# Optimization experiments

Hardware: AMD Instinct MI355X
Metric: run time of the kernel (lower is better)

## Reference

```python
import jax, jax.numpy as jnp
import numpy as np

EPS = 1e-8

def setup_inputs() -> dict:
    key = jax.random.key(0)
    k1, k2 = jax.random.split(key)
    B, C, H, W = 8, 21, 512, 512
    inp = jax.random.normal(k1, (B, C, H, W), dtype=jnp.float32)
    target = jax.random.uniform(k2, (B, C, H, W), dtype=jnp.float32)
    return {"input": inp, "target": target}

def reference(input, target):
    B, C, H, W = input.shape
    # argmax over class dim -> [B, H, W]
    pred = jnp.argmax(input, axis=1)
    # one-hot of prediction, flattened over spatial dims -> [B, HW, C]
    h = jax.nn.one_hot(pred.reshape(B, H * W), C, dtype=input.dtype)
    # target flattened over spatial dims -> [B, C, HW]
    y = target.reshape(B, C, H * W)
    # cm[b, i, j] = sum_n y[b, i, n] * h[b, n, j]  -> [B, C, C]
    cm = jnp.einsum('bin,bnj->bij', y, h)
    # row-normalize by target mass per class, then mean over batch -> [C, C]
    cm = cm / (jnp.sum(y, axis=2, keepdims=True) + EPS)
    return jnp.mean(cm, axis=0)
```

## Files before the change

### kernel.cpp

```cpp
#include <hip/hip_runtime.h>
#include <math.h>

#define NC 21
#define NB 8
#define HW (512*512)
#define EPS 1e-8f
#define NREP 8
#define TPB 256
#define G4 2
#define F4_PER_BLOCK (TPB * G4)
#define TILES_PER_IMG (HW / 4 / F4_PER_BLOCK)
#define NBLK (NB * TILES_PER_IMG)
#define PSTRIDE 512

typedef float f32x4 __attribute__((ext_vector_type(4)));


#define UPD(val, cc, mm, jj) \
    if ((val) > (mm) || ((val) == (mm) && (cc) < (jj))) { (mm) = (val); (jj) = (cc); }

template <bool PARTIAL>
__global__ __launch_bounds__(TPB) void cm_accum(const float* __restrict__ input,
                                                const float* __restrict__ target,
                                                float* __restrict__ cm ,
                                                float* __restrict__ partial ) {
    __shared__ float scm[NREP][NC * NC];
    const int t = threadIdx.x;
    for (int i = t; i < NREP * NC * NC; i += TPB) ((float*)scm)[i] = 0.0f;
    __syncthreads();

    const int bid  = blockIdx.x;
    const int b    = bid / TILES_PER_IMG;
    const int tile = bid % TILES_PER_IMG;
    const int rot  = bid % NC;

    const f32x4* ip = (const f32x4*)(input  + (size_t)b * NC * HW);
    const f32x4* tp = (const f32x4*)(target + (size_t)b * NC * HW);
    const int plane4 = HW / 4;
    const int q0 = tile * F4_PER_BLOCK + t;

    f32x4 mA, mB;
    mA.x = mA.y = mA.z = mA.w = -INFINITY;
    mB.x = mB.y = mB.z = mB.w = -INFINITY;
    int jAx = NC, jAy = NC, jAz = NC, jAw = NC;
    int jBx = NC, jBy = NC, jBz = NC, jBw = NC;

    int c = rot;
    f32x4 curA = __builtin_nontemporal_load(ip + (size_t)c * plane4 + q0);
    f32x4 curB = __builtin_nontemporal_load(ip + (size_t)c * plane4 + q0 + TPB);
    f32x4 nxtA = {}, nxtB = {};
    for (int cc = 0; cc < NC; ++cc) {
        const int cn = (c + 1 == NC) ? 0 : c + 1;
        if (cc < NC - 1) {
            nxtA = __builtin_nontemporal_load(ip + (size_t)cn * plane4 + q0);
            nxtB = __builtin_nontemporal_load(ip + (size_t)cn * plane4 + q0 + TPB);
        }
        __builtin_amdgcn_sched_barrier(0);
        UPD(curA.x, c, mA.x, jAx); UPD(curA.y, c, mA.y, jAy);
        UPD(curA.z, c, mA.z, jAz); UPD(curA.w, c, mA.w, jAw);
        UPD(curB.x, c, mB.x, jBx); UPD(curB.y, c, mB.y, jBy);
        UPD(curB.z, c, mB.z, jBz); UPD(curB.w, c, mB.w, jBw);
        curA = nxtA; curB = nxtB;
        c = cn;
    }

    float* my = scm[t & (NREP - 1)];
    c = rot;
    curA = __builtin_nontemporal_load(tp + (size_t)c * plane4 + q0);
    curB = __builtin_nontemporal_load(tp + (size_t)c * plane4 + q0 + TPB);
    for (int cc = 0; cc < NC; ++cc) {
        const int cn = (c + 1 == NC) ? 0 : c + 1;
        if (cc < NC - 1) {
            nxtA = __builtin_nontemporal_load(tp + (size_t)cn * plane4 + q0);
            nxtB = __builtin_nontemporal_load(tp + (size_t)cn * plane4 + q0 + TPB);
        }
        __builtin_amdgcn_sched_barrier(0);
        const int row = c * NC;
        atomicAdd(&my[row + jAx], curA.x);
        atomicAdd(&my[row + jAy], curA.y);
        atomicAdd(&my[row + jAz], curA.z);
        atomicAdd(&my[row + jAw], curA.w);
        atomicAdd(&my[row + jBx], curB.x);
        atomicAdd(&my[row + jBy], curB.y);
        atomicAdd(&my[row + jBz], curB.z);
        atomicAdd(&my[row + jBw], curB.w);
        curA = nxtA; curB = nxtB;
        c = cn;
    }
    __syncthreads();

    if (PARTIAL) {
        float* pout = partial + (size_t)bid * PSTRIDE;
        for (int i = t; i < PSTRIDE; i += TPB) {
            float s = 0.0f;
            if (i < NC * NC) {
                #pragma unroll
                for (int r = 0; r < NREP; ++r) s += scm[r][i];
            }
            pout[i] = s;
        }
    } else {
        for (int i = t; i < NC * NC; i += TPB) {
            float s = 0.0f;
            #pragma unroll
            for (int r = 0; r < NREP; ++r) s += scm[r][i];
            atomicAdd(&cm[b * NC * NC + i], s);
        }
    }
}

__global__ __launch_bounds__(256) void cm_reduce(const float* __restrict__ partial,
                                                 float* __restrict__ cm) {
    const int b = blockIdx.x, t = threadIdx.x;
    const float* p = partial + (size_t)b * TILES_PER_IMG * PSTRIDE;
    float s0 = 0.0f, s1 = 0.0f;
    #pragma unroll 8
    for (int s = 0; s < TILES_PER_IMG; ++s) {
        s0 += p[(size_t)s * PSTRIDE + t];
        s1 += p[(size_t)s * PSTRIDE + t + 256];
    }
    cm[b * NC * NC + t] = s0;
    if (t + 256 < NC * NC) cm[b * NC * NC + t + 256] = s1;
}

__global__ __launch_bounds__(512) void cm_final(const float* __restrict__ cm,
                                                float* __restrict__ out) {
    __shared__ float rs[NB * NC];
    const int t = threadIdx.x;
    if (t < NB * NC) {
        const int b = t / NC, i = t % NC;
        float s = 0.0f;
        for (int j = 0; j < NC; ++j) s += cm[b * NC * NC + i * NC + j];
        rs[t] = s + EPS;
    }
    __syncthreads();
    if (t < NC * NC) {
        const int i = t / NC;
        float acc = 0.0f;
        for (int b = 0; b < NB; ++b) acc += cm[b * NC * NC + t] / rs[b * NC + i];
        out[t] = acc * (1.0f / NB);
    }
}

extern "C" void kernel_launch(void* const* d_in, const int* in_sizes, int n_in,
                              void* d_out, int out_size, void* d_ws, size_t ws_size,
                              hipStream_t stream) {
    const float* input  = (const float*)d_in[0];
    const float* target = (const float*)d_in[1];
    float* out = (float*)d_out;

    const size_t partial_floats = (size_t)NBLK * PSTRIDE;
    const size_t need = (partial_floats + NB * NC * NC) * sizeof(float);

    if (ws_size >= need) {
        float* partial = (float*)d_ws;
        float* cm      = partial + partial_floats;
        cm_accum<true><<<NBLK, TPB, 0, stream>>>(input, target, cm, partial);
        cm_reduce<<<NB, 256, 0, stream>>>(partial, cm);
        cm_final<<<1, 512, 0, stream>>>(cm, out);
    } else {
        float* cm = (float*)d_ws;
        hipMemsetAsync(cm, 0, NB * NC * NC * sizeof(float), stream);
        cm_accum<false><<<NBLK, TPB, 0, stream>>>(input, target, cm, nullptr);
        cm_final<<<1, 512, 0, stream>>>(cm, out);
    }
}
```

Measured before the change: 516.4 us.

## Stage input and target planes into LDS via global_load_lds in chunks

Replaces per-thread register-prefetched nontemporal vector loads with direct global-to-LDS staging of all 21 class planes per 128-float4 chunk, processing four chunks per block. Each thread then reads two floats per class from LDS for the argmax and the atomic accumulation, and the number of shared histogram replicas is halved. This aims to raise memory-level parallelism by issuing all planes at once, but it adds a full vmcnt(0) wait plus several block barriers per chunk, which serializes loading and compute and removes the old overlap.

```diff
diff --git a/kernel.cpp b/kernel.cpp
--- a/kernel.cpp
+++ b/kernel.cpp
@@ -5,11 +5,12 @@
 #define NB 8
 #define HW (512*512)
 #define EPS 1e-8f
-#define NREP 8
+#define NREP 4
 #define TPB 256
-#define G4 2
-#define F4_PER_BLOCK (TPB * G4)
-#define TILES_PER_IMG (HW / 4 / F4_PER_BLOCK)
+#define CHUNK4 128
+#define CHUNKS_PER_BLK 4
+#define BLK4 (CHUNK4 * CHUNKS_PER_BLK)
+#define TILES_PER_IMG ((HW/4) / BLK4)
 #define NBLK (NB * TILES_PER_IMG)
 #define PSTRIDE 512
 
@@ -19,75 +20,68 @@
 #define UPD(val, cc, mm, jj) \
     if ((val) > (mm) || ((val) == (mm) && (cc) < (jj))) { (mm) = (val); (jj) = (cc); }
 
+__device__ __forceinline__ void stage_plane(const f32x4* gsrc, f32x4* lds_uniform, int lane) {
+    __builtin_amdgcn_global_load_lds(
+        (const __attribute__((address_space(1))) void*)(gsrc + lane),
+        (__attribute__((address_space(3))) void*)(uintptr_t)lds_uniform,
+        16, 0, 0);
+    __builtin_amdgcn_global_load_lds(
+        (const __attribute__((address_space(1))) void*)(gsrc + 64 + lane),
+        (__attribute__((address_space(3))) void*)(uintptr_t)(lds_uniform + 64),
+        16, 0, 0);
+}
+
 template <bool PARTIAL>
 __global__ __launch_bounds__(TPB) void cm_accum(const float* __restrict__ input,
                                                 const float* __restrict__ target,
                                                 float* __restrict__ cm ,
                                                 float* __restrict__ partial ) {
+    __shared__ f32x4 stage[NC][CHUNK4];
     __shared__ float scm[NREP][NC * NC];
     const int t = threadIdx.x;
+    const int wave = t >> 6, lane = t & 63;
     for (int i = t; i < NREP * NC * NC; i += TPB) ((float*)scm)[i] = 0.0f;
-    __syncthreads();
 
     const int bid  = blockIdx.x;
     const int b    = bid / TILES_PER_IMG;
     const int tile = bid % TILES_PER_IMG;
-    const int rot  = bid % NC;
-
     const f32x4* ip = (const f32x4*)(input  + (size_t)b * NC * HW);
     const f32x4* tp = (const f32x4*)(target + (size_t)b * NC * HW);
     const int plane4 = HW / 4;
-    const int q0 = tile * F4_PER_BLOCK + t;
 
-    f32x4 mA, mB;
-    mA.x = mA.y = mA.z = mA.w = -INFINITY;
-    mB.x = mB.y = mB.z = mB.w = -INFINITY;
-    int jAx = NC, jAy = NC, jAz = NC, jAw = NC;
-    int jBx = NC, jBy = NC, jBz = NC, jBw = NC;
+    for (int ch = 0; ch < CHUNKS_PER_BLK; ++ch) {
+        const int q0 = tile * BLK4 + ch * CHUNK4;
 
-    int c = rot;
-    f32x4 curA = __builtin_nontemporal_load(ip + (size_t)c * plane4 + q0);
-    f32x4 curB = __builtin_nontemporal_load(ip + (size_t)c * plane4 + q0 + TPB);
-    f32x4 nxtA = {}, nxtB = {};
-    for (int cc = 0; cc < NC; ++cc) {
-        const int cn = (c + 1 == NC) ? 0 : c + 1;
-        if (cc < NC - 1) {
-            nxtA = __builtin_nontemporal_load(ip + (size_t)cn * plane4 + q0);
-            nxtB = __builtin_nontemporal_load(ip + (size_t)cn * plane4 + q0 + TPB);
+        for (int c = wave; c < NC; c += 4)
+            stage_plane(ip + (size_t)c * plane4 + q0, &stage[c][0], lane);
+        asm volatile("s_waitcnt vmcnt(0)" ::: "memory");
+        __syncthreads();
+
+        float m0 = -INFINITY, m1 = -INFINITY;
+        int j0 = NC, j1 = NC;
+        #pragma unroll
+        for (int c = 0; c < NC; ++c) {
+            const float* s = (const float*)&stage[c][0];
+            const float v0 = s[2 * t], v1 = s[2 * t + 1];
+            UPD(v0, c, m0, j0);
+            UPD(v1, c, m1, j1);
         }
-        __builtin_amdgcn_sched_barrier(0);
-        UPD(curA.x, c, mA.x, jAx); UPD(curA.y, c, mA.y, jAy);
-        UPD(curA.z, c, mA.z, jAz); UPD(curA.w, c, mA.w, jAw);
-        UPD(curB.x, c, mB.x, jBx); UPD(curB.y, c, mB.y, jBy);
-        UPD(curB.z, c, mB.z, jBz); UPD(curB.w, c, mB.w, jBw);
-        curA = nxtA; curB = nxtB;
-        c = cn;
+        __syncthreads();
+
+        for (int c = wave; c < NC; c += 4)
+            stage_plane(tp + (size_t)c * plane4 + q0, &stage[c][0], lane);
+        asm volatile("s_waitcnt vmcnt(0)" ::: "memory");
+        __syncthreads();
+
+        float* my = scm[t & (NREP - 1)];
+        #pragma unroll
+        for (int c = 0; c < NC; ++c) {
+            const float* s = (const float*)&stage[c][0];
+            atomicAdd(&my[c * NC + j0], s[2 * t]);
+            atomicAdd(&my[c * NC + j1], s[2 * t + 1]);
+        }
+        __syncthreads();
     }
-
-    float* my = scm[t & (NREP - 1)];
-    c = rot;
-    curA = __builtin_nontemporal_load(tp + (size_t)c * plane4 + q0);
-    curB = __builtin_nontemporal_load(tp + (size_t)c * plane4 + q0 + TPB);
-    for (int cc = 0; cc < NC; ++cc) {
-        const int cn = (c + 1 == NC) ? 0 : c + 1;
-        if (cc < NC - 1) {
-            nxtA = __builtin_nontemporal_load(tp + (size_t)cn * plane4 + q0);
-            nxtB = __builtin_nontemporal_load(tp + (size_t)cn * plane4 + q0 + TPB);
-        }
-        __builtin_amdgcn_sched_barrier(0);
-        const int row = c * NC;
-        atomicAdd(&my[row + jAx], curA.x);
-        atomicAdd(&my[row + jAy], curA.y);
-        atomicAdd(&my[row + jAz], curA.z);
-        atomicAdd(&my[row + jAw], curA.w);
-        atomicAdd(&my[row + jBx], curB.x);
-        atomicAdd(&my[row + jBy], curB.y);
-        atomicAdd(&my[row + jBz], curB.z);
-        atomicAdd(&my[row + jBw], curB.w);
-        curA = nxtA; curB = nxtB;
-        c = cn;
-    }
-    __syncthreads();
 
     if (PARTIAL) {
         float* pout = partial + (size_t)bid * PSTRIDE;
```

New measurement: 564.9 us. 9.4% more time.
